# Performance work log

Hardware: AMD Instinct MI355X
Metric: run time of the kernel (lower is better)

The kernel has to match this reference:

```python
import jax, jax.numpy as jnp
import numpy as np

NTOKENS = 500000
NSAMPLED = 8192
NHID = 256
BATCH = 8192


def setup_inputs() -> dict:
    key = jax.random.key(0)
    k1, k2, k3, k4, k5, k6, k7 = jax.random.split(key, 7)
    inputs = jax.random.normal(k1, (BATCH, NHID), dtype=jnp.float32)
    labels = jax.random.randint(k2, (BATCH,), 0, NTOKENS, dtype=jnp.int64)
    sample_ids = jax.random.randint(k3, (NSAMPLED,), 0, NTOKENS, dtype=jnp.int64)
    true_log_freq = jax.random.uniform(k4, (BATCH,), dtype=jnp.float32)
    sample_log_freq = jax.random.uniform(k5, (NSAMPLED,), dtype=jnp.float32)
    # Learned params: nn.Linear(nhid, ntokens) -> weight [ntokens, nhid], bias [ntokens]
    bound = 1.0 / np.sqrt(NHID)
    weight = jax.random.uniform(k6, (NTOKENS, NHID), dtype=jnp.float32, minval=-bound, maxval=bound)
    bias = jax.random.uniform(k7, (NTOKENS,), dtype=jnp.float32, minval=-bound, maxval=bound)
    return {
        "inputs": inputs,
        "labels": labels,
        "sample_ids": sample_ids,
        "true_log_freq": true_log_freq,
        "sample_log_freq": sample_log_freq,
        "weight": weight,
        "bias": bias,
    }


def reference(inputs, labels, sample_ids, true_log_freq, sample_log_freq, weight, bias):
    # Gather rows for true labels and sampled negatives
    true_weights = weight[labels]          # [B, nhid]
    true_bias = bias[labels]               # [B]
    sample_weights = weight[sample_ids]    # [S, nhid]
    sample_bias = bias[sample_ids]         # [S]

    # true logits: rowwise dot product + bias, minus log-freq correction
    true_logits = jnp.sum(inputs * true_weights, axis=1) + true_bias - true_log_freq  # [B]
    # sample logits: small GEMM against gathered rows, minus log-freq correction
    sample_logits = jnp.einsum("bd,sd->bs", inputs, sample_weights) + sample_bias - sample_log_freq  # [B, S]

    logits = jnp.concatenate([true_logits[:, None], sample_logits], axis=1)  # [B, 1+S]
    new_targets = jnp.zeros((inputs.shape[0],), dtype=jnp.int32)
    return logits, new_targets
```

## Files before the change

kernel.cpp:

```cpp
#include <hip/hip_runtime.h>
#include <hip/hip_bf16.h>

#define NTOKENS 500000
#define NSAMPLED 8192
#define NHID 256
#define BATCH 8192
#define LROW 8193
#define OUT_TAIL ((size_t)BATCH * LROW)

typedef short s16x8 __attribute__((ext_vector_type(8)));
typedef float f32x4 __attribute__((ext_vector_type(4)));
typedef unsigned short u16;

static __device__ __forceinline__ u16 f2bf(float f) {
  unsigned u = __float_as_uint(f);
  return (u16)((u + 0x7fffu + ((u >> 16) & 1u)) >> 16);
}

static __device__ __forceinline__ s16x8 pack8(float4 v0, float4 v1) {
  s16x8 o;
  o[0] = (short)f2bf(v0.x); o[1] = (short)f2bf(v0.y);
  o[2] = (short)f2bf(v0.z); o[3] = (short)f2bf(v0.w);
  o[4] = (short)f2bf(v1.x); o[5] = (short)f2bf(v1.y);
  o[6] = (short)f2bf(v1.z); o[7] = (short)f2bf(v1.w);
  return o;
}

static __device__ __forceinline__ void gload_lds16(const void* g, void* l) {
  __builtin_amdgcn_global_load_lds(
      (const __attribute__((address_space(1))) void*)g,
      (__attribute__((address_space(3))) void*)l, 16, 0, 0);
}

__global__ void k_prep(const float* __restrict__ inputs, const int* __restrict__ labels,
                       const int* __restrict__ sample_ids, const float* __restrict__ tfreq,
                       const float* __restrict__ sfreq, const float* __restrict__ weight,
                       const float* __restrict__ bias, u16* __restrict__ outA,
                       u16* __restrict__ outB, float* __restrict__ colconst,
                       float* __restrict__ out) {
  int bid = blockIdx.x;
  int t = threadIdx.x;
  if (bid < 1024) {
    size_t idx = ((size_t)bid * 256 + t) * 8;
    const float4* p = (const float4*)(inputs + idx);
    *(s16x8*)(outA + idx) = pack8(p[0], p[1]);
  } else if (bid < 2048) {
    int r = (bid - 1024) * 8 + (t >> 5);
    int l = t & 31;
    int s = sample_ids[r];
    const float* src = weight + (size_t)s * NHID + l * 8;
    *(s16x8*)(outB + (size_t)r * NHID + l * 8) =
        pack8(((const float4*)src)[0], ((const float4*)src)[1]);
    if (l == 0) colconst[r] = bias[s] - sfreq[r];
  } else {
    int bb = bid - 2048;
    int w = t >> 6, lane = t & 63;
    int b = bb * 4 + w;
    int lab = labels[b];
    const float4 x = *(const float4*)(inputs + (size_t)b * NHID + lane * 4);
    const float4 ww = *(const float4*)(weight + (size_t)lab * NHID + lane * 4);
    float s = x.x * ww.x + x.y * ww.y + x.z * ww.z + x.w * ww.w;
    #pragma unroll
    for (int off = 32; off; off >>= 1) s += __shfl_down(s, off, 64);
    if (lane == 0) out[(size_t)b * LROW] = s + bias[lab] - tfreq[b];
    int tid = bb * 256 + t;
    if (tid < BATCH) out[OUT_TAIL + tid] = 0.0f;
  }
}

__global__ __launch_bounds__(512, 4) void k_gemm(const u16* __restrict__ A,
                                                 const u16* __restrict__ B,
                                                 const float* __restrict__ colconst,
                                                 float* __restrict__ out) {
  __shared__ u16 lA[128 * 64];
  __shared__ u16 lB[256 * 64];
  int t = threadIdx.x;
  int lane = t & 63;
  int w = t >> 6;
  int bid = blockIdx.x;
  int xcd = bid & 7, i = bid >> 3;
  int brow = (xcd >> 1) * 16 + (i >> 4);
  int bcol = (xcd & 1) * 16 + (i & 15);
  int wr = w >> 1, wc = w & 1;
  const int l15 = lane & 15;
  const int lhi = lane >> 4;

  f32x4 acc[2][8];
  #pragma unroll
  for (int a = 0; a < 2; ++a)
    #pragma unroll
    for (int b = 0; b < 8; ++b) acc[a][b] = (f32x4){0.f, 0.f, 0.f, 0.f};

  const u16* Abase = A + (size_t)brow * 128 * NHID;
  const u16* Bbase = B + (size_t)bcol * 256 * NHID;

  for (int kt = 0; kt < 4; ++kt) {
    #pragma unroll
    for (int j = 0; j < 2; ++j) {
      int chunk = w * 128 + j * 64 + lane;
      int row = chunk >> 3;
      int cs = (chunk & 7) ^ (row & 7);
      gload_lds16(Abase + (size_t)row * NHID + kt * 64 + cs * 8,
                  lA + (size_t)(w * 128 + j * 64) * 8);
    }
    #pragma unroll
    for (int j = 0; j < 4; ++j) {
      int chunk = w * 256 + j * 64 + lane;
      int row = chunk >> 3;
      int cs = (chunk & 7) ^ (row & 7);
      gload_lds16(Bbase + (size_t)row * NHID + kt * 64 + cs * 8,
                  lB + (size_t)(w * 256 + j * 64) * 8);
    }
    __syncthreads();
    #pragma unroll
    for (int ks = 0; ks < 2; ++ks) {
      int kc = ks * 4 + lhi;
      s16x8 af[2];
      #pragma unroll
      for (int mi = 0; mi < 2; ++mi) {
        int row = wr * 32 + mi * 16 + l15;
        af[mi] = *(const s16x8*)(lA + row * 64 + ((kc ^ (row & 7)) * 8));
      }
      #pragma unroll
      for (int ni = 0; ni < 8; ++ni) {
        int row = wc * 128 + ni * 16 + l15;
        s16x8 bf = *(const s16x8*)(lB + row * 64 + ((kc ^ (row & 7)) * 8));
        #pragma unroll
        for (int mi = 0; mi < 2; ++mi)
          acc[mi][ni] = __builtin_amdgcn_mfma_f32_16x16x32_bf16(af[mi], bf, acc[mi][ni], 0, 0, 0);
      }
    }
    __syncthreads();
  }

  int grow0 = brow * 128 + wr * 32;
  int gcol0 = bcol * 256 + wc * 128;
  float cc[8];
  #pragma unroll
  for (int ni = 0; ni < 8; ++ni) cc[ni] = colconst[gcol0 + ni * 16 + l15];
  #pragma unroll
  for (int mi = 0; mi < 2; ++mi) {
    #pragma unroll
    for (int r = 0; r < 4; ++r) {
      size_t rbase = (size_t)(grow0 + mi * 16 + lhi * 4 + r) * LROW + 1;
      #pragma unroll
      for (int ni = 0; ni < 8; ++ni)
        out[rbase + gcol0 + ni * 16 + l15] = acc[mi][ni][r] + cc[ni];
    }
  }
}

extern "C" void kernel_launch(void* const* d_in, const int* in_sizes, int n_in,
                              void* d_out, int out_size, void* d_ws, size_t ws_size,
                              hipStream_t stream) {
  const float* inputs          = (const float*)d_in[0];
  const int*   labels          = (const int*)d_in[1];
  const int*   sample_ids      = (const int*)d_in[2];
  const float* true_log_freq   = (const float*)d_in[3];
  const float* sample_log_freq = (const float*)d_in[4];
  const float* weight          = (const float*)d_in[5];
  const float* bias            = (const float*)d_in[6];
  float* out = (float*)d_out;

  u16* wsA = (u16*)d_ws;
  u16* wsB = wsA + (size_t)BATCH * NHID;
  float* colconst = (float*)(wsB + (size_t)NSAMPLED * NHID);

  hipLaunchKernelGGL(k_prep, dim3(4096), dim3(256), 0, stream,
                     inputs, labels, sample_ids, true_log_freq, sample_log_freq,
                     weight, bias, wsA, wsB, colconst, out);
  hipLaunchKernelGGL(k_gemm, dim3(2048), dim3(512), 0, stream, wsA, wsB, colconst, out);
}
```

Before: 85.56 us.

## Restructure GEMM into persistent row-block slabs streaming column chunks with full-K tiles

The GEMM is reorganized so that each of 512 blocks keeps a 32-row A tile covering all of K in LDS and loops over 32 chunks of 128 sampled columns, loading the full-K B chunk each time. Each chunk is computed and written out before the next. The aim is to make the output writes, which dominate this memory-bound problem, more contiguous per block and to avoid re-staging A. In exchange, each chunk loads B and then waits at a barrier without any double buffering, and each wave does much less MFMA work per load, so latency may be exposed.

```diff
diff --git a/kernel.cpp b/kernel.cpp
--- a/kernel.cpp
+++ b/kernel.cpp
@@ -72,81 +72,67 @@
                                                  const u16* __restrict__ B,
                                                  const float* __restrict__ colconst,
                                                  float* __restrict__ out) {
-  __shared__ u16 lA[128 * 64];
-  __shared__ u16 lB[256 * 64];
+  __shared__ u16 lA[32 * 256];
+  __shared__ u16 lB[128 * 256];
   int t = threadIdx.x;
   int lane = t & 63;
   int w = t >> 6;
+  const int l15 = lane & 15;
+  const int lhi = lane >> 4;
   int bid = blockIdx.x;
   int xcd = bid & 7, i = bid >> 3;
-  int brow = (xcd >> 1) * 16 + (i >> 4);
-  int bcol = (xcd & 1) * 16 + (i & 15);
-  int wr = w >> 1, wc = w & 1;
-  const int l15 = lane & 15;
-  const int lhi = lane >> 4;
+  int slab = xcd >> 2;
+  int brow = (xcd & 3) * 64 + i;
+  int wr = w >> 2;
+  int wc = w & 3;
 
-  f32x4 acc[2][8];
   #pragma unroll
-  for (int a = 0; a < 2; ++a)
+  for (int j = 0; j < 2; ++j) {
+    int idx = (w * 2 + j) * 64 + lane;
+    int row = idx >> 5, c = idx & 31;
+    int cs = c ^ (row & 7);
+    gload_lds16(A + (size_t)(brow * 32 + row) * NHID + cs * 8, lA + (w * 2 + j) * 512);
+  }
+
+  for (int ch = 0; ch < 32; ++ch) {
+    int colbase = slab * 4096 + ch * 128;
     #pragma unroll
-    for (int b = 0; b < 8; ++b) acc[a][b] = (f32x4){0.f, 0.f, 0.f, 0.f};
-
-  const u16* Abase = A + (size_t)brow * 128 * NHID;
-  const u16* Bbase = B + (size_t)bcol * 256 * NHID;
-
-  for (int kt = 0; kt < 4; ++kt) {
-    #pragma unroll
-    for (int j = 0; j < 2; ++j) {
-      int chunk = w * 128 + j * 64 + lane;
-      int row = chunk >> 3;
-      int cs = (chunk & 7) ^ (row & 7);
-      gload_lds16(Abase + (size_t)row * NHID + kt * 64 + cs * 8,
-                  lA + (size_t)(w * 128 + j * 64) * 8);
-    }
-    #pragma unroll
-    for (int j = 0; j < 4; ++j) {
-      int chunk = w * 256 + j * 64 + lane;
-      int row = chunk >> 3;
-      int cs = (chunk & 7) ^ (row & 7);
-      gload_lds16(Bbase + (size_t)row * NHID + kt * 64 + cs * 8,
-                  lB + (size_t)(w * 256 + j * 64) * 8);
+    for (int j = 0; j < 8; ++j) {
+      int idx = (w * 8 + j) * 64 + lane;
+      int col = idx >> 5, c = idx & 31;
+      int cs = c ^ (col & 7);
+      gload_lds16(B + (size_t)(colbase + col) * NHID + cs * 8, lB + (w * 8 + j) * 512);
     }
     __syncthreads();
+
+    f32x4 acc[2];
+    acc[0] = (f32x4){0.f, 0.f, 0.f, 0.f};
+    acc[1] = (f32x4){0.f, 0.f, 0.f, 0.f};
     #pragma unroll
-    for (int ks = 0; ks < 2; ++ks) {
-      int kc = ks * 4 + lhi;
-      s16x8 af[2];
+    for (int ks = 0; ks < 8; ++ks) {
+      int c = ks * 4 + lhi;
+      int ra = wr * 16 + l15;
+      s16x8 af = *(const s16x8*)(lA + ra * 256 + ((c ^ (ra & 7)) * 8));
       #pragma unroll
-      for (int mi = 0; mi < 2; ++mi) {
-        int row = wr * 32 + mi * 16 + l15;
-        af[mi] = *(const s16x8*)(lA + row * 64 + ((kc ^ (row & 7)) * 8));
-      }
-      #pragma unroll
-      for (int ni = 0; ni < 8; ++ni) {
-        int row = wc * 128 + ni * 16 + l15;
-        s16x8 bf = *(const s16x8*)(lB + row * 64 + ((kc ^ (row & 7)) * 8));
-        #pragma unroll
-        for (int mi = 0; mi < 2; ++mi)
-          acc[mi][ni] = __builtin_amdgcn_mfma_f32_16x16x32_bf16(af[mi], bf, acc[mi][ni], 0, 0, 0);
+      for (int ni = 0; ni < 2; ++ni) {
+        int rb = wc * 32 + ni * 16 + l15;
+        s16x8 bf = *(const s16x8*)(lB + rb * 256 + ((c ^ (rb & 7)) * 8));
+        acc[ni] = __builtin_amdgcn_mfma_f32_16x16x32_bf16(af, bf, acc[ni], 0, 0, 0);
       }
     }
-    __syncthreads();
-  }
 
-  int grow0 = brow * 128 + wr * 32;
-  int gcol0 = bcol * 256 + wc * 128;
-  float cc[8];
-  #pragma unroll
-  for (int ni = 0; ni < 8; ++ni) cc[ni] = colconst[gcol0 + ni * 16 + l15];
-  #pragma unroll
-  for (int mi = 0; mi < 2; ++mi) {
+    int gcol0 = colbase + wc * 32;
+    float cc[2];
+    #pragma unroll
+    for (int ni = 0; ni < 2; ++ni) cc[ni] = colconst[gcol0 + ni * 16 + l15];
     #pragma unroll
     for (int r = 0; r < 4; ++r) {
-      size_t rbase = (size_t)(grow0 + mi * 16 + lhi * 4 + r) * LROW + 1;
+      size_t rbase = (size_t)(brow * 32 + wr * 16 + lhi * 4 + r) * LROW + 1;
       #pragma unroll
-      for (int ni = 0; ni < 8; ++ni)
-        out[rbase + gcol0 + ni * 16 + l15] = acc[mi][ni][r] + cc[ni];
+      for (int ni = 0; ni < 2; ++ni)
+        out[rbase + gcol0 + ni * 16 + l15] = acc[ni][r] + cc[ni];
     }
+    __syncthreads();
   }
 }
 
@@ -169,5 +155,5 @@
   hipLaunchKernelGGL(k_prep, dim3(4096), dim3(256), 0, stream,
                      inputs, labels, sample_ids, true_log_freq, sample_log_freq,
                      weight, bias, wsA, wsB, colconst, out);
-  hipLaunchKernelGGL(k_gemm, dim3(2048), dim3(512), 0, stream, wsA, wsB, colconst, out);
+  hipLaunchKernelGGL(k_gemm, dim3(512), dim3(512), 0, stream, wsA, wsB, colconst, out);
 }
```

Measured after the change: 100.8 us. 17.8% more time.
